# Performance work log

Hardware: AMD Instinct MI355X
Metric: run time of the kernel (lower is better)

The kernel has to match this reference:

```python
import jax, jax.numpy as jnp
import numpy as np

BN_EPS = 1e-5


def setup_inputs() -> dict:
    key = jax.random.key(0)
    ks = jax.random.split(key, 12)
    N, E = 100000, 400000
    node_in, hidden, L = 32, 128, 4
    x = jax.random.normal(ks[0], (N, node_in), dtype=jnp.float32)
    edge_index = jax.random.randint(ks[1], (2, E), 0, N, dtype=jnp.int32)
    s = 1.0 / np.sqrt(node_in)
    emb_W = jax.random.uniform(ks[2], (node_in, hidden), minval=-s, maxval=s, dtype=jnp.float32)
    emb_b = jax.random.uniform(ks[3], (hidden,), minval=-s, maxval=s, dtype=jnp.float32)
    s1 = 1.0 / np.sqrt(hidden)
    s2 = 1.0 / np.sqrt(2 * hidden)
    W1 = jax.random.uniform(ks[4], (L, hidden, 2 * hidden), minval=-s1, maxval=s1, dtype=jnp.float32)
    b1 = jax.random.uniform(ks[5], (L, 2 * hidden), minval=-s1, maxval=s1, dtype=jnp.float32)
    W2 = jax.random.uniform(ks[6], (L, 2 * hidden, hidden), minval=-s2, maxval=s2, dtype=jnp.float32)
    b2 = jax.random.uniform(ks[7], (L, hidden), minval=-s2, maxval=s2, dtype=jnp.float32)
    gamma = jnp.ones((L, hidden), dtype=jnp.float32)
    beta = jnp.zeros((L, hidden), dtype=jnp.float32)
    return {"x": x, "edge_index": edge_index, "emb_W": emb_W, "emb_b": emb_b,
            "W1": W1, "b1": b1, "W2": W2, "b2": b2, "gamma": gamma, "beta": beta}


def reference(x, edge_index, emb_W, emb_b, W1, b1, W2, b2, gamma, beta):
    # Node embedding: [N, node_in] @ [node_in, H] -> [N, H]
    h = x @ emb_W + emb_b
    src, dst = edge_index[0], edge_index[1]
    N = h.shape[0]
    L = W1.shape[0]
    for l in range(L):
        # GINConv (eps=0): sum-aggregate neighbor features then add self
        agg = jax.ops.segment_sum(h[src], dst, num_segments=N)  # [N, H]
        z = h + agg
        # 2-layer MLP: H -> 2H -> H with ReLU
        z = jax.nn.relu(z @ W1[l] + b1[l]) @ W2[l] + b2[l]
        # BatchNorm1d over nodes (training-mode batch statistics)
        mean = jnp.mean(z, axis=0)
        var = jnp.var(z, axis=0)
        z = (z - mean) * jax.lax.rsqrt(var + BN_EPS) * gamma[l] + beta[l]
        # ReLU (dropout is identity in eval mode)
        h = jax.nn.relu(z)
    return h
```

## Files before the change

kernel.cpp:

```cpp
#include <hip/hip_runtime.h>

#define H 128
#define H2 256
#define NODE_IN 32
#define BN_EPS 1e-5f

typedef __bf16 bf16x8 __attribute__((ext_vector_type(8)));
typedef __bf16 bf16x4 __attribute__((ext_vector_type(4)));
typedef float f32x4 __attribute__((ext_vector_type(4)));

#define MFMA(a, b, c) __builtin_amdgcn_mfma_f32_16x16x32_bf16(a, b, c, 0, 0, 0)

__global__ __launch_bounds__(256) void convert_weights_kernel(
    const float* __restrict__ W1, const float* __restrict__ W2,
    const float* __restrict__ embW, char* __restrict__ Ws, int L)
{
    int idx = blockIdx.x * 256 + threadIdx.x;
    int per = H * H2;
    int total = L * per;
    if (idx < total) {
        int l = idx / per, r = idx % per;
        int k = r / H2, n = r % H2;
        int c = k >> 3, e = k & 7;
        size_t off = (size_t)l * 131072 + n * 256 + (((c ^ (n & 7)) << 4)) + e * 2;
        *(__bf16*)(Ws + off) = (__bf16)W1[idx];
    } else if (idx < 2 * total) {
        int j = idx - total;
        int l = j / per, r = j % per;
        int k = r / H, n = r % H;
        int c = k >> 3, e = k & 7;
        size_t off = (size_t)l * 131072 + 65536 + n * 512 + (((c ^ (n & 7)) << 4)) + e * 2;
        *(__bf16*)(Ws + off) = (__bf16)W2[j];
    } else if (idx < 2 * total + H * NODE_IN) {
        int j = idx - 2 * total;
        int k = j / H, c = j % H;
        size_t off = (size_t)L * 131072 + c * 64 + k * 2;
        *(__bf16*)(Ws + off) = (__bf16)embW[j];
    }
}

__global__ __launch_bounds__(512) void embed_kernel(
    const float* __restrict__ x, const char* __restrict__ Wse,
    const float* __restrict__ bias, __bf16* __restrict__ h, int N)
{
    int tid = threadIdx.x;
    int w = tid >> 6, lane = tid & 63;
    int l15 = lane & 15, kg = lane >> 4;

    bf16x8 aw[8];
#pragma unroll
    for (int nt = 0; nt < 8; ++nt)
        aw[nt] = *(const bf16x8*)(Wse + (nt * 16 + l15) * 64 + kg * 16);

    int r = (blockIdx.x * 8 + w) * 16 + l15;
    bool ok = (r < N);

    bf16x8 xb = {};
    if (ok) {
        float4 v0 = *(const float4*)&x[(size_t)r * NODE_IN + kg * 8];
        float4 v1 = *(const float4*)&x[(size_t)r * NODE_IN + kg * 8 + 4];
        xb[0] = (__bf16)v0.x; xb[1] = (__bf16)v0.y;
        xb[2] = (__bf16)v0.z; xb[3] = (__bf16)v0.w;
        xb[4] = (__bf16)v1.x; xb[5] = (__bf16)v1.y;
        xb[6] = (__bf16)v1.z; xb[7] = (__bf16)v1.w;
    }

    __bf16* hr = h + (size_t)r * H;
#pragma unroll
    for (int nt = 0; nt < 8; ++nt) {
        f32x4 acc = {0.f, 0.f, 0.f, 0.f};
        acc = MFMA(aw[nt], xb, acc);
        if (ok) {
            float4 bb = *(const float4*)&bias[nt * 16 + kg * 4];
            bf16x4 hv;
            hv[0] = (__bf16)(acc[0] + bb.x);
            hv[1] = (__bf16)(acc[1] + bb.y);
            hv[2] = (__bf16)(acc[2] + bb.z);
            hv[3] = (__bf16)(acc[3] + bb.w);
            *(bf16x4*)(hr + nt * 16 + kg * 4) = hv;
        }
    }
}

__global__ __launch_bounds__(256) void hist_kernel(
    const int* __restrict__ dst, int* __restrict__ deg, int E)
{
    int e = blockIdx.x * 256 + threadIdx.x;
    if (e < E) atomicAdd(&deg[dst[e]], 1);
}

__global__ __launch_bounds__(256) void scan_partial_kernel(
    const int* __restrict__ deg, int* __restrict__ bsum, int N)
{
    __shared__ int red[256];
    int b = blockIdx.x, t = threadIdx.x;
    int base = b * 2048 + t * 8;
    int s = 0;
#pragma unroll
    for (int i = 0; i < 8; ++i) { int idx = base + i; if (idx < N) s += deg[idx]; }
    red[t] = s;
    __syncthreads();
    for (int d = 128; d > 0; d >>= 1) {
        if (t < d) red[t] += red[t + d];
        __syncthreads();
    }
    if (t == 0) bsum[b] = red[0];
}

__global__ __launch_bounds__(256) void scan_bsum_kernel(
    int* __restrict__ bsum, int* __restrict__ total, int numB)
{
    __shared__ int ts[256];
    int t = threadIdx.x;
    int v = (t < numB) ? bsum[t] : 0;
    ts[t] = v;
    __syncthreads();
    for (int d = 1; d < 256; d <<= 1) {
        int u = (t >= d) ? ts[t - d] : 0;
        __syncthreads();
        ts[t] += u;
        __syncthreads();
    }
    if (t < numB) bsum[t] = ts[t] - v;
    if (t == 255) *total = ts[255];
}

__global__ __launch_bounds__(256) void scan_apply_kernel(
    const int* __restrict__ deg, const int* __restrict__ bsum,
    int* __restrict__ offp, int* __restrict__ cursor, int N)
{
    __shared__ int ts[256];
    int b = blockIdx.x, t = threadIdx.x;
    int base = b * 2048 + t * 8;
    int loc[8];
    int s = 0;
#pragma unroll
    for (int i = 0; i < 8; ++i) {
        int idx = base + i;
        loc[i] = (idx < N) ? deg[idx] : 0;
        s += loc[i];
    }
    ts[t] = s;
    __syncthreads();
    for (int d = 1; d < 256; d <<= 1) {
        int u = (t >= d) ? ts[t - d] : 0;
        __syncthreads();
        ts[t] += u;
        __syncthreads();
    }
    int run = bsum[b] + ts[t] - s;
#pragma unroll
    for (int i = 0; i < 8; ++i) {
        int idx = base + i;
        if (idx < N) { offp[idx] = run; cursor[idx] = run; }
        run += loc[i];
    }
}

__global__ __launch_bounds__(256) void fill_kernel(
    const int* __restrict__ src, const int* __restrict__ dst,
    int* __restrict__ cursor, int* __restrict__ srclist, int E)
{
    int e = blockIdx.x * 256 + threadIdx.x;
    if (e < E) {
        int pos = atomicAdd(&cursor[dst[e]], 1);
        srclist[pos] = src[e];
    }
}

template <int BN>
__global__ __launch_bounds__(256) void gather_kernel(
    const __bf16* __restrict__ hin, const float* __restrict__ ss,
    const int* __restrict__ offp, const int* __restrict__ srclist,
    __bf16* __restrict__ zg, int N)
{
    int gid = blockIdx.x * 256 + threadIdx.x;
    int v = gid >> 4;
    if (v >= N) return;
    int c16 = gid & 15;
    float sc[8], sh[8];
    if (BN) {
#pragma unroll
        for (int j = 0; j < 8; ++j) { sc[j] = ss[c16 * 8 + j]; sh[j] = ss[H + c16 * 8 + j]; }
    }
    float acc[8];
    bf16x8 sv = *(const bf16x8*)(hin + (size_t)v * H + c16 * 8);
#pragma unroll
    for (int j = 0; j < 8; ++j) {
        float f = (float)sv[j];
        acc[j] = BN ? fmaxf(f * sc[j] + sh[j], 0.f) : f;
    }
    int i0 = offp[v], i1 = offp[v + 1];
    int i = i0;
    for (; i + 3 < i1; i += 4) {
        int s0 = srclist[i], s1 = srclist[i + 1];
        int s2 = srclist[i + 2], s3 = srclist[i + 3];
        bf16x8 u0 = *(const bf16x8*)(hin + (size_t)s0 * H + c16 * 8);
        bf16x8 u1 = *(const bf16x8*)(hin + (size_t)s1 * H + c16 * 8);
        bf16x8 u2 = *(const bf16x8*)(hin + (size_t)s2 * H + c16 * 8);
        bf16x8 u3 = *(const bf16x8*)(hin + (size_t)s3 * H + c16 * 8);
#pragma unroll
        for (int j = 0; j < 8; ++j) {
            float f0 = (float)u0[j], f1 = (float)u1[j];
            float f2 = (float)u2[j], f3 = (float)u3[j];
            if (BN) {
                f0 = fmaxf(f0 * sc[j] + sh[j], 0.f);
                f1 = fmaxf(f1 * sc[j] + sh[j], 0.f);
                f2 = fmaxf(f2 * sc[j] + sh[j], 0.f);
                f3 = fmaxf(f3 * sc[j] + sh[j], 0.f);
            }
            acc[j] += (f0 + f1) + (f2 + f3);
        }
    }
    for (; i < i1; ++i) {
        int s0 = srclist[i];
        bf16x8 u0 = *(const bf16x8*)(hin + (size_t)s0 * H + c16 * 8);
#pragma unroll
        for (int j = 0; j < 8; ++j) {
            float f0 = (float)u0[j];
            if (BN) f0 = fmaxf(f0 * sc[j] + sh[j], 0.f);
            acc[j] += f0;
        }
    }
    bf16x8 o;
#pragma unroll
    for (int j = 0; j < 8; ++j) o[j] = (__bf16)acc[j];
    *(bf16x8*)(zg + (size_t)v * H + c16 * 8) = o;
}

__device__ __forceinline__ uint32_t pack_relu2(float x, float y) {
    __bf16 a = (__bf16)fmaxf(x, 0.f), b = (__bf16)fmaxf(y, 0.f);
    return (uint32_t)__builtin_bit_cast(uint16_t, a) |
           ((uint32_t)__builtin_bit_cast(uint16_t, b) << 16);
}

__global__ __launch_bounds__(512, 4) void mlp_fused_kernel(
    const __bf16* __restrict__ zg, __bf16* __restrict__ zpb,
    const char* __restrict__ Ws, const float* __restrict__ b1l,
    const float* __restrict__ b2l, float* __restrict__ spart, int N)
{
    __shared__ __align__(16) char hl[32768];
    __shared__ float sstat[256];

    int tid = threadIdx.x;
    int w = tid >> 6, lane = tid & 63;
    int l15 = lane & 15, kg = lane >> 4;
    const int xsw = (l15 & 7) << 4;
    int t0 = blockIdx.x * 4;

    if (tid < 256) sstat[tid] = 0.f;

    {
        bf16x8 aW1[2][4];
#pragma unroll
        for (int nt = 0; nt < 2; ++nt)
#pragma unroll
            for (int kk = 0; kk < 4; ++kk)
                aW1[nt][kk] = *(const bf16x8*)(
                    Ws + (w * 32 + nt * 16 + l15) * 256 + ((((kk * 4 + kg) << 4)) ^ xsw));
        float4 bb1[2];
#pragma unroll
        for (int nt = 0; nt < 2; ++nt)
            bb1[nt] = *(const float4*)&b1l[w * 32 + nt * 16 + kg * 4];

#pragma unroll 1
        for (int i = 0; i < 4; ++i) {
            int r = (t0 + i) * 16 + l15;
            bool ok = (r < N);
            bf16x8 zb[4];
            const __bf16* zr = zg + (size_t)r * H + kg * 8;
#pragma unroll
            for (int kk = 0; kk < 4; ++kk) {
                bf16x8 v = {};
                if (ok) v = *(const bf16x8*)(zr + kk * 32);
                zb[kk] = v;
            }
            int row = i * 16 + l15;
#pragma unroll
            for (int nt = 0; nt < 2; ++nt) {
                f32x4 a = {0.f, 0.f, 0.f, 0.f};
                a = MFMA(aW1[nt][0], zb[0], a);
                a = MFMA(aW1[nt][1], zb[1], a);
                a = MFMA(aW1[nt][2], zb[2], a);
                a = MFMA(aW1[nt][3], zb[3], a);
                uint32_t p0 = pack_relu2(a[0] + bb1[nt].x, a[1] + bb1[nt].y);
                uint32_t p1 = pack_relu2(a[2] + bb1[nt].z, a[3] + bb1[nt].w);
                int chunk = (w * 4 + nt * 2 + (kg >> 1)) ^ (l15 & 7);
                uint32_t* dstp = (uint32_t*)(hl + row * 512 + chunk * 16 + (kg & 1) * 8);
                dstp[0] = p0;
                dstp[1] = p1;
            }
        }
    }

    bf16x8 aW2[8];
#pragma unroll
    for (int kk = 0; kk < 8; ++kk)
        aW2[kk] = *(const bf16x8*)(
            Ws + 65536 + (w * 16 + l15) * 512 + ((((kk * 4 + kg) << 4)) ^ xsw));
    float4 bb2 = *(const float4*)&b2l[w * 16 + kg * 4];

    __syncthreads();

    float ps0 = 0.f, ps1 = 0.f, ps2 = 0.f, ps3 = 0.f;
    float pq0 = 0.f, pq1 = 0.f, pq2 = 0.f, pq3 = 0.f;
#pragma unroll 1
    for (int i = 0; i < 4; ++i) {
        int r = (t0 + i) * 16 + l15;
        bool ok = (r < N);
        int row = i * 16 + l15;
        bf16x8 bd[8];
#pragma unroll
        for (int kk = 0; kk < 8; ++kk)
            bd[kk] = *(const bf16x8*)(hl + row * 512 + ((((kk * 4 + kg) << 4)) ^ xsw));
        f32x4 c = {0.f, 0.f, 0.f, 0.f};
#pragma unroll
        for (int kk = 0; kk < 8; ++kk) c = MFMA(aW2[kk], bd[kk], c);
        if (ok) {
            float v0 = c[0] + bb2.x, v1 = c[1] + bb2.y;
            float v2 = c[2] + bb2.z, v3 = c[3] + bb2.w;
            bf16x4 ov;
            ov[0] = (__bf16)v0; ov[1] = (__bf16)v1;
            ov[2] = (__bf16)v2; ov[3] = (__bf16)v3;
            *(bf16x4*)(zpb + (size_t)r * H + w * 16 + kg * 4) = ov;
            ps0 += v0; pq0 += v0 * v0;
            ps1 += v1; pq1 += v1 * v1;
            ps2 += v2; pq2 += v2 * v2;
            ps3 += v3; pq3 += v3 * v3;
        }
    }

    ps0 += __shfl_xor(ps0, 1, 64); ps0 += __shfl_xor(ps0, 2, 64);
    ps0 += __shfl_xor(ps0, 4, 64); ps0 += __shfl_xor(ps0, 8, 64);
    ps1 += __shfl_xor(ps1, 1, 64); ps1 += __shfl_xor(ps1, 2, 64);
    ps1 += __shfl_xor(ps1, 4, 64); ps1 += __shfl_xor(ps1, 8, 64);
    ps2 += __shfl_xor(ps2, 1, 64); ps2 += __shfl_xor(ps2, 2, 64);
    ps2 += __shfl_xor(ps2, 4, 64); ps2 += __shfl_xor(ps2, 8, 64);
    ps3 += __shfl_xor(ps3, 1, 64); ps3 += __shfl_xor(ps3, 2, 64);
    ps3 += __shfl_xor(ps3, 4, 64); ps3 += __shfl_xor(ps3, 8, 64);
    pq0 += __shfl_xor(pq0, 1, 64); pq0 += __shfl_xor(pq0, 2, 64);
    pq0 += __shfl_xor(pq0, 4, 64); pq0 += __shfl_xor(pq0, 8, 64);
    pq1 += __shfl_xor(pq1, 1, 64); pq1 += __shfl_xor(pq1, 2, 64);
    pq1 += __shfl_xor(pq1, 4, 64); pq1 += __shfl_xor(pq1, 8, 64);
    pq2 += __shfl_xor(pq2, 1, 64); pq2 += __shfl_xor(pq2, 2, 64);
    pq2 += __shfl_xor(pq2, 4, 64); pq2 += __shfl_xor(pq2, 8, 64);
    pq3 += __shfl_xor(pq3, 1, 64); pq3 += __shfl_xor(pq3, 2, 64);
    pq3 += __shfl_xor(pq3, 4, 64); pq3 += __shfl_xor(pq3, 8, 64);
    if (l15 == 0) {
        int cb = w * 16 + kg * 4;
        sstat[cb + 0] = ps0; sstat[cb + 1] = ps1;
        sstat[cb + 2] = ps2; sstat[cb + 3] = ps3;
        sstat[H + cb + 0] = pq0; sstat[H + cb + 1] = pq1;
        sstat[H + cb + 2] = pq2; sstat[H + cb + 3] = pq3;
    }
    __syncthreads();
    if (tid < 256) spart[(size_t)blockIdx.x * 256 + tid] = sstat[tid];
}

__global__ __launch_bounds__(256) void reduce_stats_kernel(
    const float* __restrict__ spart, float* __restrict__ stats, int R)
{
    int t = threadIdx.x;
    int b = blockIdx.x;
    int per = (R + gridDim.x - 1) / gridDim.x;
    int r0 = b * per, r1 = r0 + per;
    if (r1 > R) r1 = R;
    float s = 0.f;
    for (int r = r0; r < r1; ++r) s += spart[(size_t)r * 256 + t];
    atomicAdd(&stats[t], s);
}

__global__ void bn_finalize_kernel(const float* __restrict__ stats,
                                   const float* __restrict__ gamma,
                                   const float* __restrict__ beta,
                                   float* __restrict__ ss, int N)
{
    int j = threadIdx.x;
    float invN = 1.0f / (float)N;
    float mean = stats[j] * invN;
    float var = stats[H + j] * invN - mean * mean;
    float sc = gamma[j] * rsqrtf(var + BN_EPS);
    ss[j] = sc;
    ss[H + j] = beta[j] - mean * sc;
}

__global__ __launch_bounds__(256) void bn_apply_kernel(
    const __bf16* __restrict__ zpb, const float* __restrict__ ss,
    float* __restrict__ out, int N)
{
    size_t i = (size_t)blockIdx.x * 256 + threadIdx.x;
    size_t total = (size_t)N * (H / 8);
    if (i >= total) return;
    int c8 = (int)(i & (H / 8 - 1));
    bf16x8 v = *(const bf16x8*)(zpb + i * 8);
    float4 o0, o1;
    const float* scp = &ss[c8 * 8];
    const float* shp = &ss[H + c8 * 8];
    o0.x = fmaxf((float)v[0] * scp[0] + shp[0], 0.f);
    o0.y = fmaxf((float)v[1] * scp[1] + shp[1], 0.f);
    o0.z = fmaxf((float)v[2] * scp[2] + shp[2], 0.f);
    o0.w = fmaxf((float)v[3] * scp[3] + shp[3], 0.f);
    o1.x = fmaxf((float)v[4] * scp[4] + shp[4], 0.f);
    o1.y = fmaxf((float)v[5] * scp[5] + shp[5], 0.f);
    o1.z = fmaxf((float)v[6] * scp[6] + shp[6], 0.f);
    o1.w = fmaxf((float)v[7] * scp[7] + shp[7], 0.f);
    ((float4*)out)[i * 2] = o0;
    ((float4*)out)[i * 2 + 1] = o1;
}

static inline char* align_up(char* p, size_t a) {
    return (char*)(((uintptr_t)p + a - 1) & ~(uintptr_t)(a - 1));
}

extern "C" void kernel_launch(void* const* d_in, const int* in_sizes, int n_in,
                              void* d_out, int out_size, void* d_ws, size_t ws_size,
                              hipStream_t stream)
{
    const float* x    = (const float*)d_in[0];
    const int*   ei   = (const int*)d_in[1];
    const float* embW = (const float*)d_in[2];
    const float* embb = (const float*)d_in[3];
    const float* W1   = (const float*)d_in[4];
    const float* b1   = (const float*)d_in[5];
    const float* W2   = (const float*)d_in[6];
    const float* b2   = (const float*)d_in[7];
    const float* gamma= (const float*)d_in[8];
    const float* beta = (const float*)d_in[9];

    int N = in_sizes[0] / NODE_IN;
    int E = in_sizes[1] / 2;
    int L = in_sizes[4] / (H * H2);
    const int* src = ei;
    const int* dst = ei + E;

    int numB = (N + 2047) / 2048;
    int T = (N + 15) / 16;
    int nblk = (T + 3) / 4;

    char* w = (char*)d_ws;
    __bf16* zpb = (__bf16*)w;    w += (size_t)N * H * sizeof(__bf16);
    w = align_up(w, 256);
    __bf16* zgb = (__bf16*)w;    w += (size_t)N * H * sizeof(__bf16);
    w = align_up(w, 256);
    float* spart = (float*)w;    w += (size_t)nblk * 256 * sizeof(float);
    float* statsAll = (float*)w; w += (size_t)L * 2 * H * sizeof(float);
    float* ss = (float*)w;       w += 2 * H * sizeof(float);
    int* deg = (int*)w;          w += (size_t)N * sizeof(int);
    int* offp = (int*)w;         w += (size_t)(N + 1) * sizeof(int);
    int* cursor = (int*)w;       w += (size_t)N * sizeof(int);
    int* bsum = (int*)w;         w += (size_t)numB * sizeof(int);
    int* srcl = (int*)w;         w += (size_t)E * sizeof(int);
    w = align_up(w, 256);
    char* Ws = w;                w += (size_t)L * 131072 + H * NODE_IN * 2;

    float* out = (float*)d_out;
    __bf16* h0 = zpb;

    int wtotal = 2 * L * H * H2 + H * NODE_IN;
    convert_weights_kernel<<<(wtotal + 255) / 256, 256, 0, stream>>>(W1, W2, embW, Ws, L);
    embed_kernel<<<(N + 127) / 128, 512, 0, stream>>>(
        x, Ws + (size_t)L * 131072, embb, h0, N);

    hipMemsetAsync(deg, 0, (size_t)N * sizeof(int), stream);
    hipMemsetAsync(statsAll, 0, (size_t)L * 2 * H * sizeof(float), stream);

    hist_kernel<<<(E + 255) / 256, 256, 0, stream>>>(dst, deg, E);
    scan_partial_kernel<<<numB, 256, 0, stream>>>(deg, bsum, N);
    scan_bsum_kernel<<<1, 256, 0, stream>>>(bsum, offp + N, numB);
    scan_apply_kernel<<<numB, 256, 0, stream>>>(deg, bsum, offp, cursor, N);
    fill_kernel<<<(E + 255) / 256, 256, 0, stream>>>(src, dst, cursor, srcl, E);

    int ggrid = (N * 16 + 255) / 256;
    int agrid = (int)(((size_t)N * (H / 8) + 255) / 256);

    for (int l = 0; l < L; ++l) {
        float* stats = statsAll + (size_t)l * 2 * H;
        const __bf16* hin = (l == 0) ? h0 : zpb;
        if (l == 0)
            gather_kernel<0><<<ggrid, 256, 0, stream>>>(hin, nullptr, offp, srcl, zgb, N);
        else
            gather_kernel<1><<<ggrid, 256, 0, stream>>>(hin, ss, offp, srcl, zgb, N);
        mlp_fused_kernel<<<nblk, 512, 0, stream>>>(
            zgb, zpb, Ws + (size_t)l * 131072, b1 + (size_t)l * H2,
            b2 + (size_t)l * H, spart, N);
        reduce_stats_kernel<<<64, 256, 0, stream>>>(spart, stats, nblk);
        bn_finalize_kernel<<<1, H, 0, stream>>>(
            stats, gamma + (size_t)l * H, beta + (size_t)l * H, ss, N);
    }
    bn_apply_kernel<<<agrid, 256, 0, stream>>>(zpb, ss, out, N);
}
```

Before: 396.3 us.

## Fuse neighbor gather into MLP kernel via shared-memory tile with ping-pong buffers

Merges the gather/aggregation kernel into the fused MLP kernel. Each 512-thread block now aggregates its 64 rows into a swizzled LDS tile, then runs the two MFMA GEMMs from that tile. This removes the round trip of the aggregated activations through global memory and one launch per layer. Input and output are ping-ponged between two buffers so a block never overwrites rows that other blocks still gather. The cost is more LDS per block, which may lower occupancy, and irregular gather latency now sits inside the MFMA kernel.

```diff
diff --git a/kernel.cpp b/kernel.cpp
--- a/kernel.cpp
+++ b/kernel.cpp
@@ -168,77 +168,21 @@
     }
 }
 
-template <int BN>
-__global__ __launch_bounds__(256) void gather_kernel(
-    const __bf16* __restrict__ hin, const float* __restrict__ ss,
-    const int* __restrict__ offp, const int* __restrict__ srclist,
-    __bf16* __restrict__ zg, int N)
-{
-    int gid = blockIdx.x * 256 + threadIdx.x;
-    int v = gid >> 4;
-    if (v >= N) return;
-    int c16 = gid & 15;
-    float sc[8], sh[8];
-    if (BN) {
-#pragma unroll
-        for (int j = 0; j < 8; ++j) { sc[j] = ss[c16 * 8 + j]; sh[j] = ss[H + c16 * 8 + j]; }
-    }
-    float acc[8];
-    bf16x8 sv = *(const bf16x8*)(hin + (size_t)v * H + c16 * 8);
-#pragma unroll
-    for (int j = 0; j < 8; ++j) {
-        float f = (float)sv[j];
-        acc[j] = BN ? fmaxf(f * sc[j] + sh[j], 0.f) : f;
-    }
-    int i0 = offp[v], i1 = offp[v + 1];
-    int i = i0;
-    for (; i + 3 < i1; i += 4) {
-        int s0 = srclist[i], s1 = srclist[i + 1];
-        int s2 = srclist[i + 2], s3 = srclist[i + 3];
-        bf16x8 u0 = *(const bf16x8*)(hin + (size_t)s0 * H + c16 * 8);
-        bf16x8 u1 = *(const bf16x8*)(hin + (size_t)s1 * H + c16 * 8);
-        bf16x8 u2 = *(const bf16x8*)(hin + (size_t)s2 * H + c16 * 8);
-        bf16x8 u3 = *(const bf16x8*)(hin + (size_t)s3 * H + c16 * 8);
-#pragma unroll
-        for (int j = 0; j < 8; ++j) {
-            float f0 = (float)u0[j], f1 = (float)u1[j];
-            float f2 = (float)u2[j], f3 = (float)u3[j];
-            if (BN) {
-                f0 = fmaxf(f0 * sc[j] + sh[j], 0.f);
-                f1 = fmaxf(f1 * sc[j] + sh[j], 0.f);
-                f2 = fmaxf(f2 * sc[j] + sh[j], 0.f);
-                f3 = fmaxf(f3 * sc[j] + sh[j], 0.f);
-            }
-            acc[j] += (f0 + f1) + (f2 + f3);
-        }
-    }
-    for (; i < i1; ++i) {
-        int s0 = srclist[i];
-        bf16x8 u0 = *(const bf16x8*)(hin + (size_t)s0 * H + c16 * 8);
-#pragma unroll
-        for (int j = 0; j < 8; ++j) {
-            float f0 = (float)u0[j];
-            if (BN) f0 = fmaxf(f0 * sc[j] + sh[j], 0.f);
-            acc[j] += f0;
-        }
-    }
-    bf16x8 o;
-#pragma unroll
-    for (int j = 0; j < 8; ++j) o[j] = (__bf16)acc[j];
-    *(bf16x8*)(zg + (size_t)v * H + c16 * 8) = o;
-}
-
 __device__ __forceinline__ uint32_t pack_relu2(float x, float y) {
     __bf16 a = (__bf16)fmaxf(x, 0.f), b = (__bf16)fmaxf(y, 0.f);
     return (uint32_t)__builtin_bit_cast(uint16_t, a) |
            ((uint32_t)__builtin_bit_cast(uint16_t, b) << 16);
 }
 
-__global__ __launch_bounds__(512, 4) void mlp_fused_kernel(
-    const __bf16* __restrict__ zg, __bf16* __restrict__ zpb,
+template <int BN>
+__global__ __launch_bounds__(512, 4) void gin_layer_kernel(
+    const __bf16* __restrict__ hin, __bf16* __restrict__ hout,
+    const float* __restrict__ ss,
+    const int* __restrict__ offp, const int* __restrict__ srclist,
     const char* __restrict__ Ws, const float* __restrict__ b1l,
     const float* __restrict__ b2l, float* __restrict__ spart, int N)
 {
+    __shared__ __align__(16) char zt[16384];
     __shared__ __align__(16) char hl[32768];
     __shared__ float sstat[256];
 
@@ -246,50 +190,105 @@
     int w = tid >> 6, lane = tid & 63;
     int l15 = lane & 15, kg = lane >> 4;
     const int xsw = (l15 & 7) << 4;
-    int t0 = blockIdx.x * 4;
+    int r0g = blockIdx.x * 64;
 
     if (tid < 256) sstat[tid] = 0.f;
 
+    bf16x8 aW1[2][4];
+#pragma unroll
+    for (int nt = 0; nt < 2; ++nt)
+#pragma unroll
+        for (int kk = 0; kk < 4; ++kk)
+            aW1[nt][kk] = *(const bf16x8*)(
+                Ws + (w * 32 + nt * 16 + l15) * 256 + ((((kk * 4 + kg) << 4)) ^ xsw));
+    float4 bb1[2];
+#pragma unroll
+    for (int nt = 0; nt < 2; ++nt)
+        bb1[nt] = *(const float4*)&b1l[w * 32 + nt * 16 + kg * 4];
+
     {
-        bf16x8 aW1[2][4];
-#pragma unroll
-        for (int nt = 0; nt < 2; ++nt)
-#pragma unroll
-            for (int kk = 0; kk < 4; ++kk)
-                aW1[nt][kk] = *(const bf16x8*)(
-                    Ws + (w * 32 + nt * 16 + l15) * 256 + ((((kk * 4 + kg) << 4)) ^ xsw));
-        float4 bb1[2];
-#pragma unroll
-        for (int nt = 0; nt < 2; ++nt)
-            bb1[nt] = *(const float4*)&b1l[w * 32 + nt * 16 + kg * 4];
+        float sc[8], sh[8];
+        if (BN) {
+#pragma unroll
+            for (int j = 0; j < 8; ++j) {
+                sc[j] = ss[l15 * 8 + j];
+                sh[j] = ss[H + l15 * 8 + j];
+            }
+        }
+#pragma unroll
+        for (int p = 0; p < 2; ++p) {
+            int rl = w * 8 + p * 4 + kg;
+            int r = r0g + rl;
+            bf16x8 o = {};
+            if (r < N) {
+                float acc[8];
+                bf16x8 sv = *(const bf16x8*)(hin + (size_t)r * H + l15 * 8);
+#pragma unroll
+                for (int j = 0; j < 8; ++j) {
+                    float f = (float)sv[j];
+                    acc[j] = BN ? fmaxf(f * sc[j] + sh[j], 0.f) : f;
+                }
+                int i0 = offp[r], i1 = offp[r + 1];
+                int i = i0;
+                for (; i + 3 < i1; i += 4) {
+                    int s0 = srclist[i], s1 = srclist[i + 1];
+                    int s2 = srclist[i + 2], s3 = srclist[i + 3];
+                    bf16x8 u0 = *(const bf16x8*)(hin + (size_t)s0 * H + l15 * 8);
+                    bf16x8 u1 = *(const bf16x8*)(hin + (size_t)s1 * H + l15 * 8);
+                    bf16x8 u2 = *(const bf16x8*)(hin + (size_t)s2 * H + l15 * 8);
+                    bf16x8 u3 = *(const bf16x8*)(hin + (size_t)s3 * H + l15 * 8);
+#pragma unroll
+                    for (int j = 0; j < 8; ++j) {
+                        float f0 = (float)u0[j], f1 = (float)u1[j];
+                        float f2 = (float)u2[j], f3 = (float)u3[j];
+                        if (BN) {
+                            f0 = fmaxf(f0 * sc[j] + sh[j], 0.f);
+                            f1 = fmaxf(f1 * sc[j] + sh[j], 0.f);
+                            f2 = fmaxf(f2 * sc[j] + sh[j], 0.f);
+                            f3 = fmaxf(f3 * sc[j] + sh[j], 0.f);
+                        }
+                        acc[j] += (f0 + f1) + (f2 + f3);
+                    }
+                }
+                for (; i < i1; ++i) {
+                    int s0 = srclist[i];
+                    bf16x8 u0 = *(const bf16x8*)(hin + (size_t)s0 * H + l15 * 8);
+#pragma unroll
+                    for (int j = 0; j < 8; ++j) {
+                        float f0 = (float)u0[j];
+                        if (BN) f0 = fmaxf(f0 * sc[j] + sh[j], 0.f);
+                        acc[j] += f0;
+                    }
+                }
+#pragma unroll
+                for (int j = 0; j < 8; ++j) o[j] = (__bf16)acc[j];
+            }
+            int chunk = l15 ^ (rl & 7);
+            *(bf16x8*)(zt + rl * 256 + chunk * 16) = o;
+        }
+    }
+    __syncthreads();
 
 #pragma unroll 1
-        for (int i = 0; i < 4; ++i) {
-            int r = (t0 + i) * 16 + l15;
-            bool ok = (r < N);
-            bf16x8 zb[4];
-            const __bf16* zr = zg + (size_t)r * H + kg * 8;
-#pragma unroll
-            for (int kk = 0; kk < 4; ++kk) {
-                bf16x8 v = {};
-                if (ok) v = *(const bf16x8*)(zr + kk * 32);
-                zb[kk] = v;
-            }
-            int row = i * 16 + l15;
-#pragma unroll
-            for (int nt = 0; nt < 2; ++nt) {
-                f32x4 a = {0.f, 0.f, 0.f, 0.f};
-                a = MFMA(aW1[nt][0], zb[0], a);
-                a = MFMA(aW1[nt][1], zb[1], a);
-                a = MFMA(aW1[nt][2], zb[2], a);
-                a = MFMA(aW1[nt][3], zb[3], a);
-                uint32_t p0 = pack_relu2(a[0] + bb1[nt].x, a[1] + bb1[nt].y);
-                uint32_t p1 = pack_relu2(a[2] + bb1[nt].z, a[3] + bb1[nt].w);
-                int chunk = (w * 4 + nt * 2 + (kg >> 1)) ^ (l15 & 7);
-                uint32_t* dstp = (uint32_t*)(hl + row * 512 + chunk * 16 + (kg & 1) * 8);
-                dstp[0] = p0;
-                dstp[1] = p1;
-            }
+    for (int i = 0; i < 4; ++i) {
+        int rl = i * 16 + l15;
+        bf16x8 zb[4];
+#pragma unroll
+        for (int kk = 0; kk < 4; ++kk)
+            zb[kk] = *(const bf16x8*)(zt + rl * 256 + ((((kk * 4 + kg) << 4)) ^ xsw));
+#pragma unroll
+        for (int nt = 0; nt < 2; ++nt) {
+            f32x4 a = {0.f, 0.f, 0.f, 0.f};
+            a = MFMA(aW1[nt][0], zb[0], a);
+            a = MFMA(aW1[nt][1], zb[1], a);
+            a = MFMA(aW1[nt][2], zb[2], a);
+            a = MFMA(aW1[nt][3], zb[3], a);
+            uint32_t p0 = pack_relu2(a[0] + bb1[nt].x, a[1] + bb1[nt].y);
+            uint32_t p1 = pack_relu2(a[2] + bb1[nt].z, a[3] + bb1[nt].w);
+            int chunk = (w * 4 + nt * 2 + (kg >> 1)) ^ (l15 & 7);
+            uint32_t* dstp = (uint32_t*)(hl + rl * 512 + chunk * 16 + (kg & 1) * 8);
+            dstp[0] = p0;
+            dstp[1] = p1;
         }
     }
 
@@ -306,13 +305,13 @@
     float pq0 = 0.f, pq1 = 0.f, pq2 = 0.f, pq3 = 0.f;
 #pragma unroll 1
     for (int i = 0; i < 4; ++i) {
-        int r = (t0 + i) * 16 + l15;
+        int r = r0g + i * 16 + l15;
         bool ok = (r < N);
-        int row = i * 16 + l15;
+        int rl = i * 16 + l15;
         bf16x8 bd[8];
 #pragma unroll
         for (int kk = 0; kk < 8; ++kk)
-            bd[kk] = *(const bf16x8*)(hl + row * 512 + ((((kk * 4 + kg) << 4)) ^ xsw));
+            bd[kk] = *(const bf16x8*)(hl + rl * 512 + ((((kk * 4 + kg) << 4)) ^ xsw));
         f32x4 c = {0.f, 0.f, 0.f, 0.f};
 #pragma unroll
         for (int kk = 0; kk < 8; ++kk) c = MFMA(aW2[kk], bd[kk], c);
@@ -322,7 +321,7 @@
             bf16x4 ov;
             ov[0] = (__bf16)v0; ov[1] = (__bf16)v1;
             ov[2] = (__bf16)v2; ov[3] = (__bf16)v3;
-            *(bf16x4*)(zpb + (size_t)r * H + w * 16 + kg * 4) = ov;
+            *(bf16x4*)(hout + (size_t)r * H + w * 16 + kg * 4) = ov;
             ps0 += v0; pq0 += v0 * v0;
             ps1 += v1; pq1 += v1 * v1;
             ps2 += v2; pq2 += v2 * v2;
@@ -434,13 +433,12 @@
     const int* dst = ei + E;
 
     int numB = (N + 2047) / 2048;
-    int T = (N + 15) / 16;
-    int nblk = (T + 3) / 4;
+    int nblk = (N + 63) / 64;
 
     char* w = (char*)d_ws;
-    __bf16* zpb = (__bf16*)w;    w += (size_t)N * H * sizeof(__bf16);
+    __bf16* bufA = (__bf16*)w;   w += (size_t)N * H * sizeof(__bf16);
     w = align_up(w, 256);
-    __bf16* zgb = (__bf16*)w;    w += (size_t)N * H * sizeof(__bf16);
+    __bf16* bufB = (__bf16*)w;   w += (size_t)N * H * sizeof(__bf16);
     w = align_up(w, 256);
     float* spart = (float*)w;    w += (size_t)nblk * 256 * sizeof(float);
     float* statsAll = (float*)w; w += (size_t)L * 2 * H * sizeof(float);
@@ -454,12 +452,12 @@
     char* Ws = w;                w += (size_t)L * 131072 + H * NODE_IN * 2;
 
     float* out = (float*)d_out;
-    __bf16* h0 = zpb;
+    __bf16* buf[2] = {bufA, bufB};
 
     int wtotal = 2 * L * H * H2 + H * NODE_IN;
     convert_weights_kernel<<<(wtotal + 255) / 256, 256, 0, stream>>>(W1, W2, embW, Ws, L);
     embed_kernel<<<(N + 127) / 128, 512, 0, stream>>>(
-        x, Ws + (size_t)L * 131072, embb, h0, N);
+        x, Ws + (size_t)L * 131072, embb, bufA, N);
 
     hipMemsetAsync(deg, 0, (size_t)N * sizeof(int), stream);
     hipMemsetAsync(statsAll, 0, (size_t)L * 2 * H * sizeof(float), stream);
@@ -470,22 +468,25 @@
     scan_apply_kernel<<<numB, 256, 0, stream>>>(deg, bsum, offp, cursor, N);
     fill_kernel<<<(E + 255) / 256, 256, 0, stream>>>(src, dst, cursor, srcl, E);
 
-    int ggrid = (N * 16 + 255) / 256;
     int agrid = (int)(((size_t)N * (H / 8) + 255) / 256);
 
     for (int l = 0; l < L; ++l) {
         float* stats = statsAll + (size_t)l * 2 * H;
-        const __bf16* hin = (l == 0) ? h0 : zpb;
+        const __bf16* hin = buf[l & 1];
+        __bf16* hout = buf[(l + 1) & 1];
         if (l == 0)
-            gather_kernel<0><<<ggrid, 256, 0, stream>>>(hin, nullptr, offp, srcl, zgb, N);
+            gin_layer_kernel<0><<<nblk, 512, 0, stream>>>(
+                hin, hout, nullptr, offp, srcl,
+                Ws + (size_t)l * 131072, b1 + (size_t)l * H2,
+                b2 + (size_t)l * H, spart, N);
         else
-            gather_kernel<1><<<ggrid, 256, 0, stream>>>(hin, ss, offp, srcl, zgb, N);
-        mlp_fused_kernel<<<nblk, 512, 0, stream>>>(
-            zgb, zpb, Ws + (size_t)l * 131072, b1 + (size_t)l * H2,
-            b2 + (size_t)l * H, spart, N);
+            gin_layer_kernel<1><<<nblk, 512, 0, stream>>>(
+                hin, hout, ss, offp, srcl,
+                Ws + (size_t)l * 131072, b1 + (size_t)l * H2,
+                b2 + (size_t)l * H, spart, N);
         reduce_stats_kernel<<<64, 256, 0, stream>>>(spart, stats, nblk);
         bn_finalize_kernel<<<1, H, 0, stream>>>(
             stats, gamma + (size_t)l * H, beta + (size_t)l * H, ss, N);
     }
-    bn_apply_kernel<<<agrid, 256, 0, stream>>>(zpb, ss, out, N);
-}
+    bn_apply_kernel<<<agrid, 256, 0, stream>>>(buf[L & 1], ss, out, N);
+}
```

New measurement: 364.3 us. -8.1%, faster.
